# Optimization experiments

Hardware: AMD Instinct MI355X
Metric: run time of the kernel (lower is better)

Reference implementation:

```python
import jax, jax.numpy as jnp
import numpy as np

BN_EPS = 1e-5

def _batchnorm(x):
    # BatchNorm1d(affine=False) in training mode: per-feature batch stats, biased var
    m = jnp.mean(x, axis=0)
    v = jnp.var(x, axis=0)
    return (x - m) * jax.lax.rsqrt(v + BN_EPS)

def setup_inputs() -> dict:
    key = jax.random.key(0)
    ks = jax.random.split(key, 8)
    B, S, H, I = 2, 2048, 1024, 4096
    NE, NS, K = 16384, 128, 16
    return {
        "hidden_states": jax.random.normal(ks[0], (B, S, H), dtype=jnp.float32),
        "gate_w": jax.random.normal(ks[1], (I, H), dtype=jnp.float32) * 0.02,
        "up_w": jax.random.normal(ks[2], (I, H), dtype=jnp.float32) * 0.02,
        "down_w": jax.random.normal(ks[3], (H, I), dtype=jnp.float32) * 0.02,
        "router_x_w": jax.random.normal(ks[4], (NS, H), dtype=jnp.float32) * 0.02,
        "router_y_w": jax.random.normal(ks[5], (NS, H), dtype=jnp.float32) * 0.02,
        "up_embed": jax.random.normal(ks[6], (NE, H), dtype=jnp.float32) * 0.02,
        "down_embed": jax.random.normal(ks[7], (NE, H), dtype=jnp.float32) * 0.02,
        "top_k": K,
    }

def reference(hidden_states, gate_w, up_w, down_w, router_x_w, router_y_w, up_embed, down_embed, top_k):
    B, S, H = hidden_states.shape
    ns = router_x_w.shape[0]  # num_expert_sqrt
    x = hidden_states.reshape(-1, H)  # [N, H], N = B*S

    # product-key router: two grid log-softmaxes, outer-sum, global top-k
    lpx = jax.nn.log_softmax(_batchnorm(x @ router_x_w.T), axis=-1)  # [N, ns]
    lpy = jax.nn.log_softmax(_batchnorm(x @ router_y_w.T), axis=-1)  # [N, ns]
    all_scores = (lpx[:, :, None] + lpy[:, None, :]).reshape(-1, ns * ns)  # [N, ns^2]
    scores, indices = jax.lax.top_k(all_scores, top_k)  # [N, k]
    routing_weights = jnp.exp(scores)

    # per-token expert embedding gather + small bmm chain (PEER-style)
    ue = up_embed[indices]    # [N, k, H]
    de = down_embed[indices]  # [N, k, H]
    ew = jnp.einsum('nkh,nh->nk', ue, x)
    ew = jax.nn.silu(ew) * routing_weights
    experts_states = jnp.einsum('nk,nkh->nh', ew, de).reshape(B, S, H)

    # dense gated MLP
    dense = (jax.nn.silu(x @ gate_w.T) * (x @ up_w.T)) @ down_w.T
    return dense.reshape(B, S, H) + experts_states
```

## Files before the change

### kernel.cpp

```cpp
#include <hip/hip_runtime.h>

typedef float f32x4 __attribute__((ext_vector_type(4)));
typedef short bf16x8 __attribute__((ext_vector_type(8)));
typedef unsigned short u16;

#define NEG_INF (-1e30f)

__device__ __forceinline__ u16 f2bf(float f) {
    unsigned u = __builtin_bit_cast(unsigned, f);
    unsigned r = u + 0x7FFFu + ((u >> 16) & 1u);
    return (u16)(r >> 16);
}
__device__ __forceinline__ unsigned pk2(float a, float b) {
    unsigned r;
    asm("v_cvt_pk_bf16_f32 %0, %1, %2" : "=v"(r) : "v"(a), "v"(b));
    return r;
}

__device__ __forceinline__ float wave_max(float v) {
    #pragma unroll
    for (int o = 32; o > 0; o >>= 1) v = fmaxf(v, __shfl_xor(v, o, 64));
    return v;
}
__device__ __forceinline__ float wave_sum(float v) {
    #pragma unroll
    for (int o = 32; o > 0; o >>= 1) v += __shfl_xor(v, o, 64);
    return v;
}
__device__ __forceinline__ void wave_argmax(float& v, int& i) {
    #pragma unroll
    for (int o = 32; o > 0; o >>= 1) {
        float ov = __shfl_xor(v, o, 64);
        int oi = __shfl_xor(i, o, 64);
        if (ov > v || (ov == v && oi < i)) { v = ov; i = oi; }
    }
}

__device__ __forceinline__ void g2l16(const void* g, void* l) {
    __builtin_amdgcn_global_load_lds((__attribute__((address_space(1))) void*)g,
                                     (__attribute__((address_space(3))) void*)l,
                                     16, 0, 0);
}
__device__ __forceinline__ int swz8(int row, int c) { return c ^ (row & 7); }
__device__ __forceinline__ int swz4(int row, int c) { return c ^ ((row >> 1) & 3); }

template<int NTHR>
__device__ __forceinline__ void stageA64(const u16* __restrict__ src, int ld,
                                         u16* dst, int tid) {
    #pragma unroll
    for (int r = 0; r < 2; ++r) {
        int e = r * NTHR * 8 + tid * 8;
        int row = e >> 6, c = (e >> 3) & 7;
        g2l16(src + (size_t)row * ld + swz8(row, c) * 8, dst + e);
    }
}
__device__ __forceinline__ void stageA32(const u16* __restrict__ src, int ld,
                                         u16* dst, int tid) {
    #pragma unroll
    for (int r = 0; r < 2; ++r) {
        int e = r * 2048 + tid * 8;
        int row = e >> 5, c = (e >> 3) & 3;
        g2l16(src + (size_t)row * ld + swz4(row, c) * 8, dst + e);
    }
}

__device__ __forceinline__ void loadT64_256(const float* __restrict__ src, int ld,
                                            int tid, float4* v) {
    int row = tid >> 2, col = (tid & 3) * 16;
    const float* s = src + (size_t)row * ld + col;
    v[0] = *reinterpret_cast<const float4*>(s);
    v[1] = *reinterpret_cast<const float4*>(s + 4);
    v[2] = *reinterpret_cast<const float4*>(s + 8);
    v[3] = *reinterpret_cast<const float4*>(s + 12);
}
__device__ __forceinline__ void writeT64_256(const float4* v, u16* dst, int tid) {
    int row = tid >> 2, c0 = (tid & 3) * 2;
    uint4 p0 = { pk2(v[0].x, v[0].y), pk2(v[0].z, v[0].w), pk2(v[1].x, v[1].y), pk2(v[1].z, v[1].w) };
    uint4 p1 = { pk2(v[2].x, v[2].y), pk2(v[2].z, v[2].w), pk2(v[3].x, v[3].y), pk2(v[3].z, v[3].w) };
    *reinterpret_cast<uint4*>(dst + row * 64 + swz8(row, c0) * 8) = p0;
    *reinterpret_cast<uint4*>(dst + row * 64 + swz8(row, c0 + 1) * 8) = p1;
}
__device__ __forceinline__ void loadT32(const float* __restrict__ src, int ld,
                                        int tid, float4* v) {
    int row = tid >> 1, col = (tid & 1) * 16;
    const float* s = src + (size_t)row * ld + col;
    v[0] = *reinterpret_cast<const float4*>(s);
    v[1] = *reinterpret_cast<const float4*>(s + 4);
    v[2] = *reinterpret_cast<const float4*>(s + 8);
    v[3] = *reinterpret_cast<const float4*>(s + 12);
}
__device__ __forceinline__ void writeT32(const float4* v, u16* dst, int tid) {
    int row = tid >> 1, c0 = (tid & 1) * 2;
    uint4 p0 = { pk2(v[0].x, v[0].y), pk2(v[0].z, v[0].w), pk2(v[1].x, v[1].y), pk2(v[1].z, v[1].w) };
    uint4 p1 = { pk2(v[2].x, v[2].y), pk2(v[2].z, v[2].w), pk2(v[3].x, v[3].y), pk2(v[3].z, v[3].w) };
    *reinterpret_cast<uint4*>(dst + row * 32 + swz4(row, c0) * 8) = p0;
    *reinterpret_cast<uint4*>(dst + row * 32 + swz4(row, c0 + 1) * 8) = p1;
}

__device__ __forceinline__ void loadB32bf(const u16* __restrict__ src, int ld,
                                          int tid, uint4* v) {
    int row = tid >> 1, c0 = (tid & 1) * 2;
    const u16* s = src + (size_t)row * ld;
    v[0] = *reinterpret_cast<const uint4*>(s + c0 * 8);
    v[1] = *reinterpret_cast<const uint4*>(s + (c0 + 1) * 8);
}
__device__ __forceinline__ void writeB32bf(const uint4* v, u16* dst, int tid) {
    int row = tid >> 1, c0 = (tid & 1) * 2;
    *reinterpret_cast<uint4*>(dst + row * 32 + swz4(row, c0) * 8) = v[0];
    *reinterpret_cast<uint4*>(dst + row * 32 + swz4(row, c0 + 1) * 8) = v[1];
}
__device__ __forceinline__ void loadB64bf(const u16* __restrict__ src, int ld,
                                          int tid, uint4* v) {
    int row = tid >> 2, c0 = (tid & 3) * 2;
    const u16* s = src + (size_t)row * ld;
    v[0] = *reinterpret_cast<const uint4*>(s + c0 * 8);
    v[1] = *reinterpret_cast<const uint4*>(s + (c0 + 1) * 8);
}
__device__ __forceinline__ void writeB64bf(const uint4* v, u16* dst, int tid) {
    int row = tid >> 2, c0 = (tid & 3) * 2;
    *reinterpret_cast<uint4*>(dst + row * 64 + swz8(row, c0) * 8) = v[0];
    *reinterpret_cast<uint4*>(dst + row * 64 + swz8(row, c0 + 1) * 8) = v[1];
}

__device__ __forceinline__ bf16x8 frag64s(const u16* lds, int row0, int ks, int lane) {
    int row = row0 + (lane & 15);
    int c = ks * 4 + (lane >> 4);
    return *reinterpret_cast<const bf16x8*>(lds + row * 64 + swz8(row, c) * 8);
}
__device__ __forceinline__ bf16x8 frag32s(const u16* lds, int row0, int lane) {
    int row = row0 + (lane & 15);
    int c = lane >> 4;
    return *reinterpret_cast<const bf16x8*>(lds + row * 32 + swz4(row, c) * 8);
}

__global__ void conv_x(const float* __restrict__ s, u16* __restrict__ d) {
    size_t i = (size_t)blockIdx.x * 256 + threadIdx.x;
    float4 v = *reinterpret_cast<const float4*>(s + i * 4);
    uint2 pk;
    pk.x = pk2(v.x, v.y); pk.y = pk2(v.z, v.w);
    *reinterpret_cast<uint2*>(d + i * 4) = pk;
}
__global__ void conv_all(const float* __restrict__ s0, const float* __restrict__ s1,
                         const float* __restrict__ s2, const float* __restrict__ s3,
                         u16* __restrict__ d0, u16* __restrict__ d1,
                         u16* __restrict__ d2, u16* __restrict__ d3) {
    int b = blockIdx.x, t = threadIdx.x;
    int seg = b >> 10;
    const float* s = seg == 0 ? s0 : seg == 1 ? s1 : seg == 2 ? s2 : s3;
    u16* d = seg == 0 ? d0 : seg == 1 ? d1 : seg == 2 ? d2 : d3;
    int base = (b & 1023) * 256 + t;
    #pragma unroll
    for (int j = 0; j < 4; ++j) {
        size_t i = (size_t)base + (size_t)j * 262144;
        float4 v = *reinterpret_cast<const float4*>(s + i * 4);
        uint2 pk;
        pk.x = pk2(v.x, v.y); pk.y = pk2(v.z, v.w);
        *reinterpret_cast<uint2*>(d + i * 4) = pk;
    }
}

template<bool ABF>
__global__ __launch_bounds__(256, 2) void gemm_router(
    const float* __restrict__ Xf, const u16* __restrict__ Xb,
    const float* __restrict__ RX, const float* __restrict__ RY,
    float* __restrict__ R) {
    __shared__ __align__(16) u16 As[2][4096];
    __shared__ __align__(16) u16 Bs[2][4096];
    int tid = threadIdx.x, lane = tid & 63, wave = tid >> 6;
    int rowBase = blockIdx.y * 64, colBase = blockIdx.x * 64;
    const float* Bp = (blockIdx.x < 2) ? RX + (size_t)colBase * 1024
                                       : RY + (size_t)(colBase - 128) * 1024;
    int wm = (wave >> 1) * 32, wn = (wave & 1) * 32;
    f32x4 acc[2][2] = {};
    float4 av[4], bv[4];
    if constexpr (ABF) stageA64<256>(Xb + (size_t)rowBase * 1024, 1024, As[0], tid);
    else               { loadT64_256(Xf + (size_t)rowBase * 1024, 1024, tid, av);
                         writeT64_256(av, As[0], tid); }
    loadT64_256(Bp, 1024, tid, bv);
    writeT64_256(bv, Bs[0], tid);
    __syncthreads();
    int cur = 0;
    for (int t = 0; t < 16; ++t) {
        if (t < 15) {
            int k0 = (t + 1) * 64;
            if constexpr (ABF) stageA64<256>(Xb + (size_t)rowBase * 1024 + k0, 1024, As[cur ^ 1], tid);
            else               loadT64_256(Xf + (size_t)rowBase * 1024 + k0, 1024, tid, av);
            loadT64_256(Bp + k0, 1024, tid, bv);
        }
        #pragma unroll
        for (int ks = 0; ks < 2; ++ks) {
            bf16x8 af[2], bfr[2];
            #pragma unroll
            for (int i = 0; i < 2; ++i) af[i] = frag64s(As[cur], wm + i * 16, ks, lane);
            #pragma unroll
            for (int j = 0; j < 2; ++j) bfr[j] = frag64s(Bs[cur], wn + j * 16, ks, lane);
            #pragma unroll
            for (int i = 0; i < 2; ++i)
                #pragma unroll
                for (int j = 0; j < 2; ++j)
                    acc[i][j] = __builtin_amdgcn_mfma_f32_16x16x32_bf16(af[i], bfr[j], acc[i][j], 0, 0, 0);
        }
        if (t < 15) {
            if constexpr (!ABF) writeT64_256(av, As[cur ^ 1], tid);
            writeT64_256(bv, Bs[cur ^ 1], tid);
        }
        __syncthreads();
        cur ^= 1;
    }
    int rq = (lane >> 4) * 4, cq = lane & 15;
    #pragma unroll
    for (int i = 0; i < 2; ++i)
        #pragma unroll
        for (int j = 0; j < 2; ++j) {
            int col = colBase + wn + j * 16 + cq;
            #pragma unroll
            for (int r = 0; r < 4; ++r) {
                int row = rowBase + wm + i * 16 + rq + r;
                R[(size_t)row * 256 + col] = acc[i][j][r];
            }
        }
}

template<int MODE>
__global__ __launch_bounds__(256, 2) void gemm_gateup(
    const float* __restrict__ Xf, const u16* __restrict__ Xb,
    const float* __restrict__ GWf, const float* __restrict__ UWf,
    const u16* __restrict__ GWb, const u16* __restrict__ UWb,
    u16* __restrict__ H2) {
    __shared__ __align__(16) u16 As[2][4096];
    __shared__ __align__(16) u16 Gs[2][4096];
    __shared__ __align__(16) u16 Us[2][4096];
    int tid = threadIdx.x, lane = tid & 63, wave = tid >> 6;
    int b = blockIdx.x, xcd = b & 7, ii = b >> 3;
    int by = xcd * 4 + (ii >> 5), bx = ii & 31;
    int rowBase = by * 128, colBase = bx * 128;
    int wm = (wave >> 1) * 64, wn = (wave & 1) * 64;
    f32x4 accg[4][4] = {}, accu[4][4] = {};
    float4 av[4], gv[4], uv[4];
    uint4 gv2[2], uv2[2];
    if constexpr (MODE >= 1) stageA32(Xb + (size_t)rowBase * 1024, 1024, As[0], tid);
    else                     { loadT32(Xf + (size_t)rowBase * 1024, 1024, tid, av);
                               writeT32(av, As[0], tid); }
    if constexpr (MODE == 2) {
        loadB32bf(GWb + (size_t)colBase * 1024, 1024, tid, gv2);
        loadB32bf(UWb + (size_t)colBase * 1024, 1024, tid, uv2);
        writeB32bf(gv2, Gs[0], tid);
        writeB32bf(uv2, Us[0], tid);
    } else {
        loadT32(GWf + (size_t)colBase * 1024, 1024, tid, gv);
        loadT32(UWf + (size_t)colBase * 1024, 1024, tid, uv);
        writeT32(gv, Gs[0], tid);
        writeT32(uv, Us[0], tid);
    }
    __syncthreads();
    int cur = 0;
    for (int t = 0; t < 32; ++t) {
        if (t < 31) {
            int k0 = (t + 1) * 32;
            if constexpr (MODE >= 1) stageA32(Xb + (size_t)rowBase * 1024 + k0, 1024, As[cur ^ 1], tid);
            else                     loadT32(Xf + (size_t)rowBase * 1024 + k0, 1024, tid, av);
            if constexpr (MODE == 2) {
                loadB32bf(GWb + (size_t)colBase * 1024 + k0, 1024, tid, gv2);
                loadB32bf(UWb + (size_t)colBase * 1024 + k0, 1024, tid, uv2);
            } else {
                loadT32(GWf + (size_t)colBase * 1024 + k0, 1024, tid, gv);
                loadT32(UWf + (size_t)colBase * 1024 + k0, 1024, tid, uv);
            }
        }
        bf16x8 gf[4], uf[4];
        #pragma unroll
        for (int j = 0; j < 4; ++j) { gf[j] = frag32s(Gs[cur], wn + j * 16, lane);
                                      uf[j] = frag32s(Us[cur], wn + j * 16, lane); }
        #pragma unroll
        for (int i = 0; i < 4; ++i) {
            bf16x8 af = frag32s(As[cur], wm + i * 16, lane);
            #pragma unroll
            for (int j = 0; j < 4; ++j) {
                accg[i][j] = __builtin_amdgcn_mfma_f32_16x16x32_bf16(af, gf[j], accg[i][j], 0, 0, 0);
                accu[i][j] = __builtin_amdgcn_mfma_f32_16x16x32_bf16(af, uf[j], accu[i][j], 0, 0, 0);
            }
        }
        if (t < 31) {
            if constexpr (MODE == 0) writeT32(av, As[cur ^ 1], tid);
            if constexpr (MODE == 2) { writeB32bf(gv2, Gs[cur ^ 1], tid);
                                       writeB32bf(uv2, Us[cur ^ 1], tid); }
            else if constexpr (MODE < 2) { writeT32(gv, Gs[cur ^ 1], tid);
                                           writeT32(uv, Us[cur ^ 1], tid); }
        }
        __syncthreads();
        cur ^= 1;
    }
    int rq = (lane >> 4) * 4, cq = lane & 15;
    #pragma unroll
    for (int i = 0; i < 4; ++i)
        #pragma unroll
        for (int j = 0; j < 4; ++j) {
            int col = colBase + wn + j * 16 + cq;
            #pragma unroll
            for (int r = 0; r < 4; ++r) {
                int row = rowBase + wm + i * 16 + rq + r;
                float gvv = accg[i][j][r], uvv = accu[i][j][r];
                float h = (gvv / (1.f + __expf(-gvv))) * uvv;
                H2[(size_t)row * 4096 + col] = f2bf(h);
            }
        }
}

template<int DMODE>
__global__ __launch_bounds__(256, 4) void gemm_down64(
    const u16* __restrict__ H2, const float* __restrict__ DWf, const u16* __restrict__ DWb,
    float* __restrict__ Out) {
    __shared__ __align__(16) u16 As[2][4096];
    __shared__ __align__(16) u16 Bs[2][4096];
    int tid = threadIdx.x, lane = tid & 63, wave = tid >> 6;
    int b = blockIdx.x, xcd = b & 7, ii = b >> 3;
    int by = xcd * 8 + (ii >> 4), bx = ii & 15;
    int rowBase = by * 64, colBase = bx * 64;
    const u16* Ap = H2 + (size_t)rowBase * 4096;
    int wm = (wave >> 1) * 32, wn = (wave & 1) * 32;
    f32x4 acc[2][2] = {};
    float4 bv[4];
    uint4 bv2[2];
    stageA64<256>(Ap, 4096, As[0], tid);
    if constexpr (DMODE == 1) { loadB64bf(DWb + (size_t)colBase * 4096, 4096, tid, bv2);
                                writeB64bf(bv2, Bs[0], tid); }
    else                      { loadT64_256(DWf + (size_t)colBase * 4096, 4096, tid, bv);
                                writeT64_256(bv, Bs[0], tid); }
    __syncthreads();
    int cur = 0;
    for (int t = 0; t < 64; ++t) {
        if (t < 63) {
            int k0 = (t + 1) * 64;
            stageA64<256>(Ap + k0, 4096, As[cur ^ 1], tid);
            if constexpr (DMODE == 1) loadB64bf(DWb + (size_t)colBase * 4096 + k0, 4096, tid, bv2);
            else                      loadT64_256(DWf + (size_t)colBase * 4096 + k0, 4096, tid, bv);
        }
        #pragma unroll
        for (int ks = 0; ks < 2; ++ks) {
            bf16x8 af[2], bfr[2];
            #pragma unroll
            for (int i = 0; i < 2; ++i) af[i] = frag64s(As[cur], wm + i * 16, ks, lane);
            #pragma unroll
            for (int j = 0; j < 2; ++j) bfr[j] = frag64s(Bs[cur], wn + j * 16, ks, lane);
            #pragma unroll
            for (int i = 0; i < 2; ++i)
                #pragma unroll
                for (int j = 0; j < 2; ++j)
                    acc[i][j] = __builtin_amdgcn_mfma_f32_16x16x32_bf16(af[i], bfr[j], acc[i][j], 0, 0, 0);
        }
        if (t < 63) {
            if constexpr (DMODE == 1) writeB64bf(bv2, Bs[cur ^ 1], tid);
            else                      writeT64_256(bv, Bs[cur ^ 1], tid);
        }
        __syncthreads();
        cur ^= 1;
    }
    int rq = (lane >> 4) * 4, cq = lane & 15;
    #pragma unroll
    for (int i = 0; i < 2; ++i)
        #pragma unroll
        for (int j = 0; j < 2; ++j) {
            int col = colBase + wn + j * 16 + cq;
            #pragma unroll
            for (int r = 0; r < 4; ++r) {
                int row = rowBase + wm + i * 16 + rq + r;
                size_t o = (size_t)row * 1024 + col;
                Out[o] = acc[i][j][r] + Out[o];
            }
        }
}

__global__ __launch_bounds__(256) void expert_store(
    const float* __restrict__ X, const float* __restrict__ UE, const float* __restrict__ DE,
    const int* __restrict__ idxs, const float* __restrict__ wts, float* __restrict__ Out) {
    int n = blockIdx.x, tid = threadIdx.x;
    int lane = tid & 63, wave = tid >> 6;
    __shared__ float xs[1024];
    __shared__ float ews[16];
    __shared__ int sidx[16];
    __shared__ float swt[16];
    if (tid < 16) {
        sidx[tid] = min(max(idxs[n * 16 + tid], 0), 16383);
        swt[tid] = wts[n * 16 + tid];
    }
    {
        float4 v = reinterpret_cast<const float4*>(X + (size_t)n * 1024)[tid];
        *reinterpret_cast<float4*>(xs + tid * 4) = v;
    }
    __syncthreads();
    #pragma unroll
    for (int q = 0; q < 4; ++q) {
        int e = wave * 4 + q;
        const float* row = UE + (size_t)sidx[e] * 1024;
        float acc = 0.f;
        #pragma unroll
        for (int c = 0; c < 4; ++c) {
            int h = c * 256 + lane * 4;
            float4 a = *reinterpret_cast<const float4*>(row + h);
            float4 xv = *reinterpret_cast<const float4*>(xs + h);
            acc += a.x * xv.x + a.y * xv.y + a.z * xv.z + a.w * xv.w;
        }
        acc = wave_sum(acc);
        if (lane == 0) {
            float s = acc / (1.f + __expf(-acc));
            ews[e] = s * swt[e];
        }
    }
    __syncthreads();
    float4 a = make_float4(0.f, 0.f, 0.f, 0.f);
    int h = tid * 4;
    #pragma unroll
    for (int e = 0; e < 16; ++e) {
        const float* row = DE + (size_t)sidx[e] * 1024;
        float4 v = *reinterpret_cast<const float4*>(row + h);
        float w = ews[e];
        a.x += w * v.x; a.y += w * v.y;
        a.z += w * v.z; a.w += w * v.w;
    }
    reinterpret_cast<float4*>(Out + (size_t)n * 1024)[tid] = a;
}

__global__ void bn_stats(const float* __restrict__ R, float* __restrict__ stats) {
    int c = threadIdx.x;
    int r0 = blockIdx.x * 64;
    float s = 0.f, s2 = 0.f;
    for (int r = r0; r < r0 + 64; ++r) {
        float v = R[(size_t)r * 256 + c];
        s += v; s2 += v * v;
    }
    atomicAdd(&stats[c], s);
    atomicAdd(&stats[256 + c], s2);
}

__global__ __launch_bounds__(64) void router_topk(
    const float* __restrict__ R, const float* __restrict__ stats,
    int* __restrict__ idx_out, float* __restrict__ wt_out) {
    int n = blockIdx.x, lane = threadIdx.x;
    const float invN = 1.0f / 4096.0f;
    float z[4];
    #pragma unroll
    for (int p = 0; p < 4; ++p) {
        int c = p * 64 + lane;
        float mean = stats[c] * invN;
        float var = fmaxf(stats[256 + c] * invN - mean * mean, 0.f);
        float v = R[(size_t)n * 256 + c];
        z[p] = (v - mean) * rsqrtf(var + 1e-5f);
    }
    float mx = wave_max(fmaxf(z[0], z[1]));
    float sx = __logf(wave_sum(__expf(z[0] - mx) + __expf(z[1] - mx)));
    float lx0 = z[0] - mx - sx, lx1 = z[1] - mx - sx;
    float my = wave_max(fmaxf(z[2], z[3]));
    float sy = __logf(wave_sum(__expf(z[2] - my) + __expf(z[3] - my)));
    float ly0 = z[2] - my - sy, ly1 = z[3] - my - sy;

    __shared__ float tx[16], ty[16];
    __shared__ int txc[16], tyc[16];
    float v0 = lx0, v1 = lx1;
    for (int t = 0; t < 16; ++t) {
        float bv; int bc;
        if (v1 > v0) { bv = v1; bc = lane + 64; } else { bv = v0; bc = lane; }
        wave_argmax(bv, bc);
        if (lane == 0) { tx[t] = bv; txc[t] = bc; }
        if (bc == lane) v0 = NEG_INF;
        else if (bc == lane + 64) v1 = NEG_INF;
    }
    v0 = ly0; v1 = ly1;
    for (int t = 0; t < 16; ++t) {
        float bv; int bc;
        if (v1 > v0) { bv = v1; bc = lane + 64; } else { bv = v0; bc = lane; }
        wave_argmax(bv, bc);
        if (lane == 0) { ty[t] = bv; tyc[t] = bc; }
        if (bc == lane) v0 = NEG_INF;
        else if (bc == lane + 64) v1 = NEG_INF;
    }
    __syncthreads();
    float cv[4]; int ci[4];
    #pragma unroll
    for (int p = 0; p < 4; ++p) {
        int pid = p * 64 + lane;
        cv[p] = tx[pid >> 4] + ty[pid & 15];
        ci[p] = pid;
    }
    for (int t = 0; t < 16; ++t) {
        float bv = cv[0]; int bc = ci[0];
        #pragma unroll
        for (int p = 1; p < 4; ++p)
            if (cv[p] > bv) { bv = cv[p]; bc = ci[p]; }
        wave_argmax(bv, bc);
        if (lane == 0) {
            idx_out[n * 16 + t] = txc[bc >> 4] * 128 + tyc[bc & 15];
            wt_out[n * 16 + t] = __expf(bv);
        }
        #pragma unroll
        for (int p = 0; p < 4; ++p)
            if (ci[p] == bc) cv[p] = NEG_INF;
    }
}

extern "C" void kernel_launch(void* const* d_in, const int* in_sizes, int n_in,
                              void* d_out, int out_size, void* d_ws, size_t ws_size,
                              hipStream_t stream) {
    const float* x   = (const float*)d_in[0];
    const float* gw  = (const float*)d_in[1];
    const float* uw  = (const float*)d_in[2];
    const float* dw  = (const float*)d_in[3];
    const float* rxw = (const float*)d_in[4];
    const float* ryw = (const float*)d_in[5];
    const float* ue  = (const float*)d_in[6];
    const float* de  = (const float*)d_in[7];
    float* out = (float*)d_out;

    char* p = (char*)d_ws;
    float* stats = (float*)p; p += 16384;
    int*   idxb  = (int*)p;   p += 262144;
    float* wtb   = (float*)p; p += 262144;
    float* R     = (float*)p;
    u16*   H2    = (u16*)p;

    u16* xb  = (u16*)((char*)d_ws + 34095104ull);
    u16* gwb = (u16*)((char*)d_ws + 42483712ull);
    u16* uwb = (u16*)((char*)d_ws + 50872320ull);
    u16* dwb = (u16*)((char*)d_ws + 59260928ull);
    int tier = ws_size >= 67649536ull ? 2 : ws_size >= 42483712ull ? 1 : 0;

    hipMemsetAsync(stats, 0, 512 * sizeof(float), stream);
    if (tier == 2)      conv_all<<<4096, 256, 0, stream>>>(x, gw, uw, dw, xb, gwb, uwb, dwb);
    else if (tier == 1) conv_x<<<4096, 256, 0, stream>>>(x, xb);

    if (tier >= 1) gemm_router<true ><<<dim3(4, 64), 256, 0, stream>>>(x, xb, rxw, ryw, R);
    else           gemm_router<false><<<dim3(4, 64), 256, 0, stream>>>(x, (const u16*)x, rxw, ryw, R);
    bn_stats<<<64, 256, 0, stream>>>(R, stats);
    router_topk<<<4096, 64, 0, stream>>>(R, stats, idxb, wtb);
    expert_store<<<4096, 256, 0, stream>>>(x, ue, de, idxb, wtb, out);

    if (tier == 2)      gemm_gateup<2><<<1024, 256, 0, stream>>>(x, xb, gw, uw, gwb, uwb, H2);
    else if (tier == 1) gemm_gateup<1><<<1024, 256, 0, stream>>>(x, xb, gw, uw, nullptr, nullptr, H2);
    else                gemm_gateup<0><<<1024, 256, 0, stream>>>(x, (const u16*)x, gw, uw, nullptr, nullptr, H2);

    if (tier == 2) gemm_down64<1><<<1024, 256, 0, stream>>>(H2, dw, dwb, out);
    else           gemm_down64<0><<<1024, 256, 0, stream>>>(H2, dw, (const u16*)dw, out);
}
```

Baseline: 464.0 us.

## Enlarge down-projection tile to 128 rows and batch expert dot-product loads

The down-projection GEMM now computes 128x64 output tiles with each wave holding a 64x32 accumulator, launching 512 blocks instead of 1024. Each loaded weight tile is reused across twice as many rows, cutting global/LDS traffic per output, in exchange for more registers and LDS and lower occupancy (launch bound 2). The expert kernel also interleaves the four expert-row dot products per wave so their loads can be in flight together, and does a single combined shuffle reduction.

New measurement: 475.9 us. +2.6%, slower.

```diff
diff --git a/kernel.cpp b/kernel.cpp
--- a/kernel.cpp
+++ b/kernel.cpp
@@ -44,11 +44,11 @@
 __device__ __forceinline__ int swz8(int row, int c) { return c ^ (row & 7); }
 __device__ __forceinline__ int swz4(int row, int c) { return c ^ ((row >> 1) & 3); }
 
-template<int NTHR>
-__device__ __forceinline__ void stageA64(const u16* __restrict__ src, int ld,
-                                         u16* dst, int tid) {
-    #pragma unroll
-    for (int r = 0; r < 2; ++r) {
+template<int NTHR, int NROUND>
+__device__ __forceinline__ void stageA64R(const u16* __restrict__ src, int ld,
+                                          u16* dst, int tid) {
+    #pragma unroll
+    for (int r = 0; r < NROUND; ++r) {
         int e = r * NTHR * 8 + tid * 8;
         int row = e >> 6, c = (e >> 3) & 7;
         g2l16(src + (size_t)row * ld + swz8(row, c) * 8, dst + e);
@@ -173,7 +173,7 @@
     int wm = (wave >> 1) * 32, wn = (wave & 1) * 32;
     f32x4 acc[2][2] = {};
     float4 av[4], bv[4];
-    if constexpr (ABF) stageA64<256>(Xb + (size_t)rowBase * 1024, 1024, As[0], tid);
+    if constexpr (ABF) stageA64R<256, 2>(Xb + (size_t)rowBase * 1024, 1024, As[0], tid);
     else               { loadT64_256(Xf + (size_t)rowBase * 1024, 1024, tid, av);
                          writeT64_256(av, As[0], tid); }
     loadT64_256(Bp, 1024, tid, bv);
@@ -183,7 +183,7 @@
     for (int t = 0; t < 16; ++t) {
         if (t < 15) {
             int k0 = (t + 1) * 64;
-            if constexpr (ABF) stageA64<256>(Xb + (size_t)rowBase * 1024 + k0, 1024, As[cur ^ 1], tid);
+            if constexpr (ABF) stageA64R<256, 2>(Xb + (size_t)rowBase * 1024 + k0, 1024, As[cur ^ 1], tid);
             else               loadT64_256(Xf + (size_t)rowBase * 1024 + k0, 1024, tid, av);
             loadT64_256(Bp + k0, 1024, tid, bv);
         }
@@ -307,21 +307,21 @@
 }
 
 template<int DMODE>
-__global__ __launch_bounds__(256, 4) void gemm_down64(
+__global__ __launch_bounds__(256, 2) void gemm_down128(
     const u16* __restrict__ H2, const float* __restrict__ DWf, const u16* __restrict__ DWb,
     float* __restrict__ Out) {
-    __shared__ __align__(16) u16 As[2][4096];
+    __shared__ __align__(16) u16 As[2][8192];
     __shared__ __align__(16) u16 Bs[2][4096];
     int tid = threadIdx.x, lane = tid & 63, wave = tid >> 6;
     int b = blockIdx.x, xcd = b & 7, ii = b >> 3;
-    int by = xcd * 8 + (ii >> 4), bx = ii & 15;
-    int rowBase = by * 64, colBase = bx * 64;
+    int by = xcd * 4 + (ii >> 4), bx = ii & 15;
+    int rowBase = by * 128, colBase = bx * 64;
     const u16* Ap = H2 + (size_t)rowBase * 4096;
-    int wm = (wave >> 1) * 32, wn = (wave & 1) * 32;
-    f32x4 acc[2][2] = {};
+    int wm = (wave >> 1) * 64, wn = (wave & 1) * 32;
+    f32x4 acc[4][2] = {};
     float4 bv[4];
     uint4 bv2[2];
-    stageA64<256>(Ap, 4096, As[0], tid);
+    stageA64R<256, 4>(Ap, 4096, As[0], tid);
     if constexpr (DMODE == 1) { loadB64bf(DWb + (size_t)colBase * 4096, 4096, tid, bv2);
                                 writeB64bf(bv2, Bs[0], tid); }
     else                      { loadT64_256(DWf + (size_t)colBase * 4096, 4096, tid, bv);
@@ -331,19 +331,19 @@
     for (int t = 0; t < 64; ++t) {
         if (t < 63) {
             int k0 = (t + 1) * 64;
-            stageA64<256>(Ap + k0, 4096, As[cur ^ 1], tid);
+            stageA64R<256, 4>(Ap + k0, 4096, As[cur ^ 1], tid);
             if constexpr (DMODE == 1) loadB64bf(DWb + (size_t)colBase * 4096 + k0, 4096, tid, bv2);
             else                      loadT64_256(DWf + (size_t)colBase * 4096 + k0, 4096, tid, bv);
         }
         #pragma unroll
         for (int ks = 0; ks < 2; ++ks) {
-            bf16x8 af[2], bfr[2];
-            #pragma unroll
-            for (int i = 0; i < 2; ++i) af[i] = frag64s(As[cur], wm + i * 16, ks, lane);
+            bf16x8 af[4], bfr[2];
+            #pragma unroll
+            for (int i = 0; i < 4; ++i) af[i] = frag64s(As[cur], wm + i * 16, ks, lane);
             #pragma unroll
             for (int j = 0; j < 2; ++j) bfr[j] = frag64s(Bs[cur], wn + j * 16, ks, lane);
             #pragma unroll
-            for (int i = 0; i < 2; ++i)
+            for (int i = 0; i < 4; ++i)
                 #pragma unroll
                 for (int j = 0; j < 2; ++j)
                     acc[i][j] = __builtin_amdgcn_mfma_f32_16x16x32_bf16(af[i], bfr[j], acc[i][j], 0, 0, 0);
@@ -357,7 +357,7 @@
     }
     int rq = (lane >> 4) * 4, cq = lane & 15;
     #pragma unroll
-    for (int i = 0; i < 2; ++i)
+    for (int i = 0; i < 4; ++i)
         #pragma unroll
         for (int j = 0; j < 2; ++j) {
             int col = colBase + wn + j * 16 + cq;
@@ -388,23 +388,31 @@
         *reinterpret_cast<float4*>(xs + tid * 4) = v;
     }
     __syncthreads();
-    #pragma unroll
-    for (int q = 0; q < 4; ++q) {
-        int e = wave * 4 + q;
-        const float* row = UE + (size_t)sidx[e] * 1024;
-        float acc = 0.f;
-        #pragma unroll
-        for (int c = 0; c < 4; ++c) {
-            int h = c * 256 + lane * 4;
-            float4 a = *reinterpret_cast<const float4*>(row + h);
-            float4 xv = *reinterpret_cast<const float4*>(xs + h);
-            acc += a.x * xv.x + a.y * xv.y + a.z * xv.z + a.w * xv.w;
-        }
-        acc = wave_sum(acc);
-        if (lane == 0) {
-            float s = acc / (1.f + __expf(-acc));
-            ews[e] = s * swt[e];
-        }
+    const float* rows[4];
+    #pragma unroll
+    for (int q = 0; q < 4; ++q)
+        rows[q] = UE + (size_t)sidx[wave * 4 + q] * 1024;
+    float a4[4] = {0.f, 0.f, 0.f, 0.f};
+    #pragma unroll
+    for (int c = 0; c < 4; ++c) {
+        int h = c * 256 + lane * 4;
+        float4 xv = *reinterpret_cast<const float4*>(xs + h);
+        #pragma unroll
+        for (int q = 0; q < 4; ++q) {
+            float4 a = *reinterpret_cast<const float4*>(rows[q] + h);
+            a4[q] += a.x * xv.x + a.y * xv.y + a.z * xv.z + a.w * xv.w;
+        }
+    }
+    #pragma unroll
+    for (int o = 32; o > 0; o >>= 1) {
+        #pragma unroll
+        for (int q = 0; q < 4; ++q) a4[q] += __shfl_xor(a4[q], o, 64);
+    }
+    if (lane < 4) {
+        float acc = lane == 0 ? a4[0] : lane == 1 ? a4[1] : lane == 2 ? a4[2] : a4[3];
+        int e = wave * 4 + lane;
+        float s = acc / (1.f + __expf(-acc));
+        ews[e] = s * swt[e];
     }
     __syncthreads();
     float4 a = make_float4(0.f, 0.f, 0.f, 0.f);
@@ -537,6 +545,6 @@
     else if (tier == 1) gemm_gateup<1><<<1024, 256, 0, stream>>>(x, xb, gw, uw, nullptr, nullptr, H2);
     else                gemm_gateup<0><<<1024, 256, 0, stream>>>(x, (const u16*)x, gw, uw, nullptr, nullptr, H2);
 
-    if (tier == 2) gemm_down64<1><<<1024, 256, 0, stream>>>(H2, dw, dwb, out);
-    else           gemm_down64<0><<<1024, 256, 0, stream>>>(H2, dw, (const u16*)dw, out);
-}
+    if (tier == 2) gemm_down128<1><<<512, 256, 0, stream>>>(H2, dw, dwb, out);
+    else           gemm_down128<0><<<512, 256, 0, stream>>>(H2, dw, (const u16*)dw, out);
+}
```
